# Kernel optimization log

Hardware: AMD Instinct MI355X
Metric: run time of the kernel (lower is better)

Reference implementation:

```python
import jax, jax.numpy as jnp
import numpy as np

N = 10000   # num_nodes (batch=1)
E = 160000  # num edges
CIN, H, T, OUT, K = 32, 64, 12, 12, 3


def _conv1d(x, w, b, pad):
    # x: [N, C_in, T], w: [C_out, C_in, K]
    out = jax.lax.conv_general_dilated(
        x, w, window_strides=(1,), padding=[(pad, pad)],
        dimension_numbers=('NCH', 'OIH', 'NCH'))
    return out + b[None, :, None]


def _gated_tconv(x, w, b):
    # GatedTemporalConv (dropout = identity in eval)
    out = _conv1d(x, w, b, K // 2)
    P, Q = jnp.split(out, 2, axis=1)
    return P * jax.nn.sigmoid(Q)


def _gcn(x, W, b, src, dst, ew):
    # PyG GCNConv, vectorized over all T timesteps in one fused pass.
    # x: [N, C_in, T], W: [C_out, C_in]
    xt = jnp.einsum('nct,oc->not', x, W)
    loop = jnp.arange(N)
    srcl = jnp.concatenate([src, loop])
    dstl = jnp.concatenate([dst, loop])
    ewl = jnp.concatenate([ew, jnp.ones((N,), ew.dtype)])
    deg = jax.ops.segment_sum(ewl, dstl, num_segments=N)
    dis = jnp.where(deg > 0, jax.lax.rsqrt(deg), 0.0)
    norm = dis[srcl] * ewl * dis[dstl]                      # [E+N]
    msg = xt[srcl] * norm[:, None, None]                    # [E+N, C_out, T]
    out = jax.ops.segment_sum(msg, dstl, num_segments=N)    # [N, C_out, T]
    return out + b[None, :, None]


def setup_inputs() -> dict:
    key = jax.random.key(0)
    ks = jax.random.split(key, 20)
    rn = lambda k, s: jax.random.normal(k, s, jnp.float32) * 0.05
    return {
        'x': jax.random.normal(ks[0], (N, CIN, T), jnp.float32),
        'edge_index': jax.random.randint(ks[1], (2, E), 0, N),
        'edge_weight': jax.random.uniform(ks[2], (E,), jnp.float32),
        'tc1a_w': rn(ks[3], (2 * H, CIN, K)), 'tc1a_b': rn(ks[4], (2 * H,)),
        'gc1_w': rn(ks[5], (H, H)),           'gc1_b': rn(ks[6], (H,)),
        'tc1b_w': rn(ks[7], (2 * H, H, K)),   'tc1b_b': rn(ks[8], (2 * H,)),
        'tc2a_w': rn(ks[9], (2 * H, H, K)),   'tc2a_b': rn(ks[10], (2 * H,)),
        'gc2_w': rn(ks[11], (H, H)),          'gc2_b': rn(ks[12], (H,)),
        'tc2b_w': rn(ks[13], (2 * H, H, K)),  'tc2b_b': rn(ks[14], (2 * H,)),
        'fin_w': rn(ks[15], (OUT, H, T)),     'fin_b': rn(ks[16], (OUT,)),
    }


def reference(x, edge_index, edge_weight,
              tc1a_w, tc1a_b, gc1_w, gc1_b, tc1b_w, tc1b_b,
              tc2a_w, tc2a_b, gc2_w, gc2_b, tc2b_w, tc2b_b,
              fin_w, fin_b):
    src, dst = edge_index[0], edge_index[1]
    h = _gated_tconv(x, tc1a_w, tc1a_b)
    h = jax.nn.relu(_gcn(h, gc1_w, gc1_b, src, dst, edge_weight))
    h = _gated_tconv(h, tc1b_w, tc1b_b)
    h = _gated_tconv(h, tc2a_w, tc2a_b)
    h = jax.nn.relu(_gcn(h, gc2_w, gc2_b, src, dst, edge_weight))
    h = _gated_tconv(h, tc2b_w, tc2b_b)
    h = _conv1d(h, fin_w, fin_b, 0)          # [N, OUT, 1] (kernel == T)
    h = h[:, :, 0]                            # squeeze(-1)
    return h.reshape(1, N, OUT)               # batch_size = 1
```

## Files before the change

### kernel.cpp

```cpp
#include <hip/hip_runtime.h>
#include <hip/hip_bf16.h>
#include <stdint.h>

#define N_NODES 10000
#define N_EDGES 160000
#define BUCKET 128

typedef unsigned short u16;
typedef unsigned int u32;
typedef short s16v8 __attribute__((ext_vector_type(8)));
typedef float f32v4 __attribute__((ext_vector_type(4)));

__device__ __forceinline__ float bf2f(u16 v){ return __uint_as_float(((u32)v) << 16); }
__device__ __forceinline__ u16 f2bf(float f){
    u32 u = __float_as_uint(f);
    u32 r = (u + 0x7fffu + ((u >> 16) & 1u)) >> 16;
    return (u16)r;
}

struct SmallPtrs { const void* p[14]; };

__device__ __constant__ const int g_seg_off[15] = {
    0, 12288, 12416, 16512, 16576, 41152, 41280,
    65856, 65984, 70080, 70144, 94720, 94848, 104064, 104076
};
__device__ __constant__ const int g_seg_kind[14] = {
    1, 0, 0, 0, 2, 0, 2, 0, 0, 0, 2, 0, 0, 0
};

__global__ void k_convert_init(SmallPtrs ps, u16* __restrict__ dst,
                               float* deg, int* cur){
    int i = blockIdx.x * blockDim.x + threadIdx.x;
    if (i < 104076){
        int seg = 0, base = 0;
#pragma unroll
        for (int s = 0; s < 14; s++){
            if (i >= g_seg_off[s]){ seg = s; base = g_seg_off[s]; }
        }
        int li = i - base;
        float v = ((const float*)ps.p[seg])[li];
        int kind = g_seg_kind[seg];
        int dsto = li;
        if (kind){
            int CIN = (kind == 1) ? 32 : 64;
            int o = li / (3 * CIN);
            int rem = li - o * (3 * CIN);
            int c = rem / 3, d = rem - c * 3;
            dsto = d * 128 * CIN + o * CIN + c;
        }
        dst[base + dsto] = f2bf(v);
    }
    if (i < N_NODES){ deg[i] = 1.0f; cur[i] = 0; }
}

__launch_bounds__(256, 4)
__global__ void k_gconv_count(const float* __restrict__ xin, const u16* __restrict__ wg,
                              const u16* __restrict__ bg, u16* __restrict__ out,
                              const int* __restrict__ ei, const float* __restrict__ ew,
                              float* deg, int* cur, int2* __restrict__ epack){
    if (blockIdx.x >= 1250){
        int e = (blockIdx.x - 1250) * 256 + threadIdx.x;
        if (e < N_EDGES){
            int s = ei[e];
            int d = ei[N_EDGES + e];
            float wv = ew[e];
            atomicAdd(&deg[d], wv);
            int p = atomicAdd(&cur[d], 1);
            if (p < BUCKET) epack[d * BUCKET + p] = make_int2(s, __float_as_int(wv));
        }
        return;
    }
    __shared__ __attribute__((aligned(16))) u16 shbuf[6912];
    u16* xT = shbuf;
    u16* Ho = shbuf;
    int tid = threadIdx.x;
    int n0 = blockIdx.x * 8;

    int lane = tid & 63, wave = tid >> 6;
    int col = lane & 15, quad = lane >> 4;
    int o_p = wave * 16 + col, o_q = o_p + 64;

    s16v8 Bf[3][2];
#pragma unroll
    for (int pq = 0; pq < 2; pq++){
        int o = pq ? o_q : o_p;
#pragma unroll
        for (int d = 0; d < 3; d++)
            Bf[d][pq] = *(const s16v8*)(wg + d * 4096 + o * 32 + quad * 8);
    }

    for (int i = tid; i < 8 * 40; i += 256){
        int g = i / 40, c = i % 40;
        xT[g * 560 + 0 * 40 + c] = 0; xT[g * 560 + 13 * 40 + c] = 0;
    }
    {
        int g = tid >> 5, c = tid & 31;
        const float4* p = (const float4*)(xin + ((size_t)(n0 + g) * 32 + c) * 12);
        float4 v0 = p[0], v1 = p[1], v2 = p[2];
        u16* xb = xT + g * 560 + c;
        xb[1 * 40] = f2bf(v0.x);  xb[2 * 40] = f2bf(v0.y);
        xb[3 * 40] = f2bf(v0.z);  xb[4 * 40] = f2bf(v0.w);
        xb[5 * 40] = f2bf(v1.x);  xb[6 * 40] = f2bf(v1.y);
        xb[7 * 40] = f2bf(v1.z);  xb[8 * 40] = f2bf(v1.w);
        xb[9 * 40] = f2bf(v2.x);  xb[10 * 40] = f2bf(v2.y);
        xb[11 * 40] = f2bf(v2.z); xb[12 * 40] = f2bf(v2.w);
    }
    __syncthreads();

    f32v4 aP[6], aQ[6];
#pragma unroll
    for (int mt = 0; mt < 6; mt++){ aP[mt] = (f32v4)0.f; aQ[mt] = (f32v4)0.f; }
#pragma unroll
    for (int mt = 0; mt < 6; mt++){
        int m = mt * 16 + col;
        int g = m / 12, t = m - 12 * g;
#pragma unroll
        for (int d = 0; d < 3; d++){
            s16v8 a = *(const s16v8*)&xT[g * 560 + (t + d) * 40 + quad * 8];
            aP[mt] = __builtin_amdgcn_mfma_f32_16x16x32_bf16(a, Bf[d][0], aP[mt], 0, 0, 0);
            aQ[mt] = __builtin_amdgcn_mfma_f32_16x16x32_bf16(a, Bf[d][1], aQ[mt], 0, 0, 0);
        }
    }
    __syncthreads();
    float bP = bf2f(bg[o_p]), bQ = bf2f(bg[o_q]);
#pragma unroll
    for (int mt = 0; mt < 6; mt++){
#pragma unroll
        for (int r = 0; r < 4; r++){
            int m2 = mt * 16 + quad * 4 + r;
            int g = m2 / 12, t = m2 - 12 * g;
            float pv = aP[mt][r] + bP, qv = aQ[mt][r] + bQ;
            Ho[g * 864 + t * 72 + o_p] = f2bf(pv / (1.f + __expf(-qv)));
        }
    }
    __syncthreads();
    for (int i = tid; i < 768; i += 256){
        int g = i / 96, r = i % 96, t = r / 8, ch = r % 8;
        *(s16v8*)(out + (size_t)(n0 + g) * 768 + t * 64 + ch * 8) =
            *(const s16v8*)&Ho[g * 864 + t * 72 + ch * 8];
    }
}

__global__ void k_norm(const float* __restrict__ deg, const int* __restrict__ cur,
                       int2* __restrict__ ep){
    int i = blockIdx.x * blockDim.x + threadIdx.x;
    int n = i >> 7, slot = i & 127;
    if (n >= N_NODES) return;
    int cnt = cur[n]; if (cnt > BUCKET) cnt = BUCKET;
    if (slot < cnt){
        int2 e = ep[(size_t)n * BUCKET + slot];
        float w = __int_as_float(e.y) * rsqrtf(deg[e.x]) * rsqrtf(deg[n]);
        ep[(size_t)n * BUCKET + slot].y = __float_as_int(w);
    }
}

__launch_bounds__(256, 4)
__global__ void k_gather(const u16* __restrict__ src, const float* __restrict__ deg,
                         const int* __restrict__ cur, const int2* __restrict__ ep,
                         u16* __restrict__ z){
    int slice = blockIdx.x & 7;
    int nb = blockIdx.x >> 3;
    int tid = threadIdx.x;
    int nl = tid >> 5;
    int sub = tid & 31;
    int eg = sub >> 3;
    int l8 = sub & 7;
    int n = nb * 8 + nl;
    int base = slice * 96 + l8 * 12;

    float acc[12];
    if (eg == 0){
        float sw = 1.0f / deg[n];
        const u16* xr = src + (size_t)n * 768 + base;
#pragma unroll
        for (int k = 0; k < 3; k++){
            ushort4 v = *(const ushort4*)(xr + k * 4);
            acc[k * 4 + 0] = sw * bf2f(v.x); acc[k * 4 + 1] = sw * bf2f(v.y);
            acc[k * 4 + 2] = sw * bf2f(v.z); acc[k * 4 + 3] = sw * bf2f(v.w);
        }
    } else {
#pragma unroll
        for (int k = 0; k < 12; k++) acc[k] = 0.f;
    }

    int e = cur[n]; if (e > BUCKET) e = BUCKET;
    const int2* eb = ep + (size_t)n * BUCKET;
    int p = eg;
    for (; p + 4 < e; p += 8){
        int2 e0 = eb[p], e1 = eb[p + 4];
        float w0 = __int_as_float(e0.y), w1 = __int_as_float(e1.y);
        const u16* q0 = src + (size_t)e0.x * 768 + base;
        const u16* q1 = src + (size_t)e1.x * 768 + base;
        ushort4 a0 = *(const ushort4*)(q0);
        ushort4 a1 = *(const ushort4*)(q0 + 4);
        ushort4 a2 = *(const ushort4*)(q0 + 8);
        ushort4 c0 = *(const ushort4*)(q1);
        ushort4 c1 = *(const ushort4*)(q1 + 4);
        ushort4 c2 = *(const ushort4*)(q1 + 8);
        acc[0] = fmaf(w0, bf2f(a0.x), acc[0]); acc[1] = fmaf(w0, bf2f(a0.y), acc[1]);
        acc[2] = fmaf(w0, bf2f(a0.z), acc[2]); acc[3] = fmaf(w0, bf2f(a0.w), acc[3]);
        acc[4] = fmaf(w0, bf2f(a1.x), acc[4]); acc[5] = fmaf(w0, bf2f(a1.y), acc[5]);
        acc[6] = fmaf(w0, bf2f(a1.z), acc[6]); acc[7] = fmaf(w0, bf2f(a1.w), acc[7]);
        acc[8] = fmaf(w0, bf2f(a2.x), acc[8]); acc[9] = fmaf(w0, bf2f(a2.y), acc[9]);
        acc[10] = fmaf(w0, bf2f(a2.z), acc[10]); acc[11] = fmaf(w0, bf2f(a2.w), acc[11]);
        acc[0] = fmaf(w1, bf2f(c0.x), acc[0]); acc[1] = fmaf(w1, bf2f(c0.y), acc[1]);
        acc[2] = fmaf(w1, bf2f(c0.z), acc[2]); acc[3] = fmaf(w1, bf2f(c0.w), acc[3]);
        acc[4] = fmaf(w1, bf2f(c1.x), acc[4]); acc[5] = fmaf(w1, bf2f(c1.y), acc[5]);
        acc[6] = fmaf(w1, bf2f(c1.z), acc[6]); acc[7] = fmaf(w1, bf2f(c1.w), acc[7]);
        acc[8] = fmaf(w1, bf2f(c2.x), acc[8]); acc[9] = fmaf(w1, bf2f(c2.y), acc[9]);
        acc[10] = fmaf(w1, bf2f(c2.z), acc[10]); acc[11] = fmaf(w1, bf2f(c2.w), acc[11]);
    }
    if (p < e){
        int2 e0 = eb[p];
        float w0 = __int_as_float(e0.y);
        const u16* q0 = src + (size_t)e0.x * 768 + base;
#pragma unroll
        for (int k = 0; k < 3; k++){
            ushort4 v = *(const ushort4*)(q0 + k * 4);
            acc[k * 4 + 0] = fmaf(w0, bf2f(v.x), acc[k * 4 + 0]);
            acc[k * 4 + 1] = fmaf(w0, bf2f(v.y), acc[k * 4 + 1]);
            acc[k * 4 + 2] = fmaf(w0, bf2f(v.z), acc[k * 4 + 2]);
            acc[k * 4 + 3] = fmaf(w0, bf2f(v.w), acc[k * 4 + 3]);
        }
    }
#pragma unroll
    for (int k = 0; k < 12; k++){
        acc[k] += __shfl_xor(acc[k], 8, 64);
        acc[k] += __shfl_xor(acc[k], 16, 64);
    }
    if (eg == 0){
        u16* zo = z + (size_t)n * 768 + base;
#pragma unroll
        for (int k = 0; k < 3; k++){
            ushort4 hv;
            hv.x = f2bf(acc[k * 4 + 0]); hv.y = f2bf(acc[k * 4 + 1]);
            hv.z = f2bf(acc[k * 4 + 2]); hv.w = f2bf(acc[k * 4 + 3]);
            *(ushort4*)(zo + k * 4) = hv;
        }
    }
}

#define XIDX(g, row, c) (((g) * 14 + (row)) * 72 + (c))

template<bool LAST>
__launch_bounds__(256, 4)
__global__ void k_fused(const u16* __restrict__ z,
                        const u16* __restrict__ Wmix, const u16* __restrict__ bmix,
                        const u16* __restrict__ w1, const u16* __restrict__ b1,
                        const u16* __restrict__ w2, const u16* __restrict__ b2,
                        const u16* __restrict__ fw, const u16* __restrict__ fb,
                        u16* __restrict__ outMid, float* __restrict__ outFin){
    __shared__ __attribute__((aligned(16))) u16 bufX[8 * 14 * 72];
    __shared__ __attribute__((aligned(16))) u16 bufY[8 * 14 * 72];
    int tid = threadIdx.x;
    int n0 = blockIdx.x * 8;
    int lane = tid & 63, wave = tid >> 6;
    int col = lane & 15, quad = lane >> 4;
    int o_p = wave * 16 + col, o_q = o_p + 64;

    for (int i = tid; i < 8 * 72; i += 256){
        int g = i / 72, c = i % 72;
        bufX[XIDX(g, 0, c)] = 0; bufX[XIDX(g, 13, c)] = 0;
        bufY[XIDX(g, 0, c)] = 0; bufY[XIDX(g, 13, c)] = 0;
    }
    for (int i = tid; i < 768; i += 256){
        int g = i / 96, r = i % 96, t = r >> 3, ch = r & 7;
        *(s16v8*)&bufX[XIDX(g, 1 + t, ch * 8)] =
            *(const s16v8*)(z + (size_t)(n0 + g) * 768 + t * 64 + ch * 8);
    }
    __syncthreads();

    {
        f32v4 accm[6];
#pragma unroll
        for (int mt = 0; mt < 6; mt++) accm[mt] = (f32v4)0.f;
#pragma unroll
        for (int ks = 0; ks < 2; ks++){
            s16v8 Bm = *(const s16v8*)(Wmix + (size_t)o_p * 64 + ks * 32 + quad * 8);
#pragma unroll
            for (int mt = 0; mt < 6; mt++){
                int m = mt * 16 + col;
                int g = m / 12, t = m - 12 * g;
                s16v8 a = *(const s16v8*)&bufX[XIDX(g, 1 + t, ks * 32 + quad * 8)];
                accm[mt] = __builtin_amdgcn_mfma_f32_16x16x32_bf16(a, Bm, accm[mt], 0, 0, 0);
            }
        }
        float bm = bf2f(bmix[o_p]);
#pragma unroll
        for (int mt = 0; mt < 6; mt++){
#pragma unroll
            for (int r = 0; r < 4; r++){
                int m2 = mt * 16 + quad * 4 + r;
                int g = m2 / 12, t = m2 - 12 * g;
                bufY[XIDX(g, 1 + t, o_p)] = f2bf(fmaxf(accm[mt][r] + bm, 0.f));
            }
        }
    }
    __syncthreads();

    {
        f32v4 aP[6], aQ[6];
#pragma unroll
        for (int mt = 0; mt < 6; mt++){ aP[mt] = (f32v4)0.f; aQ[mt] = (f32v4)0.f; }
#pragma unroll
        for (int ks = 0; ks < 2; ks++){
            s16v8 Bf[3][2];
#pragma unroll
            for (int pq = 0; pq < 2; pq++){
                int o = pq ? o_q : o_p;
#pragma unroll
                for (int d = 0; d < 3; d++)
                    Bf[d][pq] = *(const s16v8*)(w1 + d * 8192 + o * 64 + ks * 32 + quad * 8);
            }
#pragma unroll
            for (int mt = 0; mt < 6; mt++){
                int m = mt * 16 + col;
                int g = m / 12, t = m - 12 * g;
#pragma unroll
                for (int d = 0; d < 3; d++){
                    s16v8 a = *(const s16v8*)&bufY[XIDX(g, t + d, ks * 32 + quad * 8)];
                    aP[mt] = __builtin_amdgcn_mfma_f32_16x16x32_bf16(a, Bf[d][0], aP[mt], 0, 0, 0);
                    aQ[mt] = __builtin_amdgcn_mfma_f32_16x16x32_bf16(a, Bf[d][1], aQ[mt], 0, 0, 0);
                }
            }
        }
        float bP = bf2f(b1[o_p]), bQ = bf2f(b1[o_q]);
#pragma unroll
        for (int mt = 0; mt < 6; mt++){
#pragma unroll
            for (int r = 0; r < 4; r++){
                int m2 = mt * 16 + quad * 4 + r;
                int g = m2 / 12, t = m2 - 12 * g;
                float pv = aP[mt][r] + bP, qv = aQ[mt][r] + bQ;
                u16 hv = f2bf(pv / (1.f + __expf(-qv)));
                if (LAST) bufX[g * 1008 + o_p * 12 + t] = hv;
                else      bufX[XIDX(g, 1 + t, o_p)] = hv;
            }
        }
    }
    __syncthreads();

    if (!LAST){
        f32v4 aP[6], aQ[6];
#pragma unroll
        for (int mt = 0; mt < 6; mt++){ aP[mt] = (f32v4)0.f; aQ[mt] = (f32v4)0.f; }
#pragma unroll
        for (int ks = 0; ks < 2; ks++){
            s16v8 Bf[3][2];
#pragma unroll
            for (int pq = 0; pq < 2; pq++){
                int o = pq ? o_q : o_p;
#pragma unroll
                for (int d = 0; d < 3; d++)
                    Bf[d][pq] = *(const s16v8*)(w2 + d * 8192 + o * 64 + ks * 32 + quad * 8);
            }
#pragma unroll
            for (int mt = 0; mt < 6; mt++){
                int m = mt * 16 + col;
                int g = m / 12, t = m - 12 * g;
#pragma unroll
                for (int d = 0; d < 3; d++){
                    s16v8 a = *(const s16v8*)&bufX[XIDX(g, t + d, ks * 32 + quad * 8)];
                    aP[mt] = __builtin_amdgcn_mfma_f32_16x16x32_bf16(a, Bf[d][0], aP[mt], 0, 0, 0);
                    aQ[mt] = __builtin_amdgcn_mfma_f32_16x16x32_bf16(a, Bf[d][1], aQ[mt], 0, 0, 0);
                }
            }
        }
        float bP = bf2f(b2[o_p]), bQ = bf2f(b2[o_q]);
#pragma unroll
        for (int mt = 0; mt < 6; mt++){
#pragma unroll
            for (int r = 0; r < 4; r++){
                int m2 = mt * 16 + quad * 4 + r;
                int g = m2 / 12, t = m2 - 12 * g;
                float pv = aP[mt][r] + bP, qv = aQ[mt][r] + bQ;
                bufY[XIDX(g, 1 + t, o_p)] = f2bf(pv / (1.f + __expf(-qv)));
            }
        }
        __syncthreads();
        for (int i = tid; i < 768; i += 256){
            int g = i / 96, r = i % 96, t = r / 8, ch = r % 8;
            *(s16v8*)(outMid + (size_t)(n0 + g) * 768 + t * 64 + ch * 8) =
                *(const s16v8*)&bufY[XIDX(g, 1 + t, ch * 8)];
        }
    } else {
        if (wave == 0){
            f32v4 accF = {0.f, 0.f, 0.f, 0.f};
            int g8 = col & 7;
#pragma unroll
            for (int ks = 0; ks < 24; ks++){
                s16v8 a = *(const s16v8*)&bufX[g8 * 1008 + ks * 32 + quad * 8];
                s16v8 bfr = {0, 0, 0, 0, 0, 0, 0, 0};
                if (col < 12)
                    bfr = *(const s16v8*)(fw + (size_t)col * 768 + ks * 32 + quad * 8);
                accF = __builtin_amdgcn_mfma_f32_16x16x32_bf16(a, bfr, accF, 0, 0, 0);
            }
            if (col < 12 && quad < 2){
                float bb = bf2f(fb[col]);
#pragma unroll
                for (int r = 0; r < 4; r++){
                    int g = quad * 4 + r;
                    outFin[(size_t)(n0 + g) * 12 + col] = accF[r] + bb;
                }
            }
        }
    }
}

static inline size_t align256(size_t x){ return (x + 255) & ~(size_t)255; }

extern "C" void kernel_launch(void* const* d_in, const int* in_sizes, int n_in,
                              void* d_out, int out_size, void* d_ws, size_t ws_size,
                              hipStream_t stream){
    const float* x  = (const float*)d_in[0];
    const int* ei   = (const int*)d_in[1];
    const float* ew = (const float*)d_in[2];

    char* w = (char*)d_ws;
    u16* bufA    = (u16*)w;  w += align256((size_t)N_NODES * 768 * sizeof(u16));
    u16* bufB    = (u16*)w;  w += align256((size_t)N_NODES * 768 * sizeof(u16));
    u16* zA      = (u16*)w;  w += align256((size_t)N_NODES * 768 * sizeof(u16));
    u16* zB      = (u16*)w;  w += align256((size_t)N_NODES * 768 * sizeof(u16));
    float* deg   = (float*)w; w += align256(N_NODES * sizeof(float));
    int* cur     = (int*)w;   w += align256(N_NODES * sizeof(int));
    int2* epack  = (int2*)w;  w += align256((size_t)N_NODES * BUCKET * sizeof(int2));
    u16* cvt     = (u16*)w;   w += align256(104076 * sizeof(u16));

    u16* tc1a_w = cvt + 0;
    u16* tc1a_b = cvt + 12288;
    u16* gc1_w  = cvt + 12416;
    u16* gc1_b  = cvt + 16512;
    u16* tc1b_w = cvt + 16576;
    u16* tc1b_b = cvt + 41152;
    u16* tc2a_w = cvt + 41280;
    u16* tc2a_b = cvt + 65856;
    u16* gc2_w  = cvt + 65984;
    u16* gc2_b  = cvt + 70080;
    u16* tc2b_w = cvt + 70144;
    u16* tc2b_b = cvt + 94720;
    u16* fin_w  = cvt + 94848;
    u16* fin_b  = cvt + 104064;

    SmallPtrs ps;
    ps.p[0]  = d_in[3];  ps.p[1]  = d_in[4];
    ps.p[2]  = d_in[5];  ps.p[3]  = d_in[6];
    ps.p[4]  = d_in[7];  ps.p[5]  = d_in[8];
    ps.p[6]  = d_in[9];  ps.p[7]  = d_in[10];
    ps.p[8]  = d_in[11]; ps.p[9]  = d_in[12];
    ps.p[10] = d_in[13]; ps.p[11] = d_in[14];
    ps.p[12] = d_in[15]; ps.p[13] = d_in[16];

    k_convert_init<<<(104076 + 255) / 256, 256, 0, stream>>>(ps, cvt, deg, cur);
    k_gconv_count<<<1250 + 625, 256, 0, stream>>>(x, tc1a_w, tc1a_b, bufA, ei, ew, deg, cur, epack);
    k_norm<<<(N_NODES * BUCKET) / 256, 256, 0, stream>>>(deg, cur, epack);

    k_gather<<<1250 * 8, 256, 0, stream>>>(bufA, deg, cur, epack, zA);
    k_fused<false><<<1250, 256, 0, stream>>>(zA, gc1_w, gc1_b, tc1b_w, tc1b_b,
                                             tc2a_w, tc2a_b, nullptr, nullptr,
                                             bufB, nullptr);
    k_gather<<<1250 * 8, 256, 0, stream>>>(bufB, deg, cur, epack, zB);
    k_fused<true><<<1250, 256, 0, stream>>>(zB, gc2_w, gc2_b, tc2b_w, tc2b_b,
                                            nullptr, nullptr, fin_w, fin_b,
                                            nullptr, (float*)d_out);
}
```

Before: 230.2 us.

## Vectorize gather loads, zero-pad edge buckets, and unroll first 24 slots unconditionally

The gather kernel now loads each neighbour row slice with one 16-byte and one 8-byte load instead of three 8-byte loads, and splits each lane's 12 channels into a contiguous 8-channel part and a 4-channel part. It accumulates with packed f32x2 math and reads edge pairs as int4. k_norm zero-fills bucket slots past the degree up to 24, so the gather can run the first 24 slots unconditionally without a bounds check, which is meant to raise memory-level parallelism. The cost is extra loads of node 0 with zero weight for low-degree nodes, plus the changed element-to-lane mapping.

```diff
diff --git a/kernel.cpp b/kernel.cpp
--- a/kernel.cpp
+++ b/kernel.cpp
@@ -5,17 +5,30 @@
 #define N_NODES 10000
 #define N_EDGES 160000
 #define BUCKET 128
+#define UNROLL_SLOTS 24
 
 typedef unsigned short u16;
 typedef unsigned int u32;
 typedef short s16v8 __attribute__((ext_vector_type(8)));
 typedef float f32v4 __attribute__((ext_vector_type(4)));
+typedef float f32v2 __attribute__((ext_vector_type(2)));
+typedef unsigned int u32v4 __attribute__((ext_vector_type(4)));
+typedef unsigned int u32v2 __attribute__((ext_vector_type(2)));
 
 __device__ __forceinline__ float bf2f(u16 v){ return __uint_as_float(((u32)v) << 16); }
 __device__ __forceinline__ u16 f2bf(float f){
     u32 u = __float_as_uint(f);
     u32 r = (u + 0x7fffu + ((u >> 16) & 1u)) >> 16;
     return (u16)r;
+}
+__device__ __forceinline__ f32v2 up2(u32 v){
+    f32v2 r;
+    r.x = __uint_as_float(v << 16);
+    r.y = __uint_as_float(v & 0xffff0000u);
+    return r;
+}
+__device__ __forceinline__ u32 pk2(float lo, float hi){
+    return (u32)f2bf(lo) | ((u32)f2bf(hi) << 16);
 }
 
 struct SmallPtrs { const void* p[14]; };
@@ -151,8 +164,34 @@
         int2 e = ep[(size_t)n * BUCKET + slot];
         float w = __int_as_float(e.y) * rsqrtf(deg[e.x]) * rsqrtf(deg[n]);
         ep[(size_t)n * BUCKET + slot].y = __float_as_int(w);
-    }
-}
+    } else if (slot < UNROLL_SLOTS){
+        ep[(size_t)n * BUCKET + slot] = make_int2(0, 0);
+    }
+}
+
+#define GATHER2(P) { \
+    int4 m = *(const int4*)(eb + (P)); \
+    const u16* q0 = src + (size_t)(u32)m.x * 768; \
+    const u16* q1 = src + (size_t)(u32)m.z * 768; \
+    u32v4 a0 = *(const u32v4*)(q0 + off1); u32v2 b0 = *(const u32v2*)(q0 + off2); \
+    u32v4 a1 = *(const u32v4*)(q1 + off1); u32v2 b1 = *(const u32v2*)(q1 + off2); \
+    f32v2 w0; w0.x = __int_as_float(m.y); w0.y = w0.x; \
+    f32v2 w1; w1.x = __int_as_float(m.w); w1.y = w1.x; \
+    acc[0] += w0 * up2(a0.x); acc[1] += w0 * up2(a0.y); \
+    acc[2] += w0 * up2(a0.z); acc[3] += w0 * up2(a0.w); \
+    acc[4] += w0 * up2(b0.x); acc[5] += w0 * up2(b0.y); \
+    acc[0] += w1 * up2(a1.x); acc[1] += w1 * up2(a1.y); \
+    acc[2] += w1 * up2(a1.z); acc[3] += w1 * up2(a1.w); \
+    acc[4] += w1 * up2(b1.x); acc[5] += w1 * up2(b1.y); }
+
+#define GATHER1(P) { \
+    int2 e0 = eb[(P)]; \
+    const u16* q0 = src + (size_t)(u32)e0.x * 768; \
+    u32v4 a0 = *(const u32v4*)(q0 + off1); u32v2 b0 = *(const u32v2*)(q0 + off2); \
+    f32v2 w0; w0.x = __int_as_float(e0.y); w0.y = w0.x; \
+    acc[0] += w0 * up2(a0.x); acc[1] += w0 * up2(a0.y); \
+    acc[2] += w0 * up2(a0.z); acc[3] += w0 * up2(a0.w); \
+    acc[4] += w0 * up2(b0.x); acc[5] += w0 * up2(b0.y); }
 
 __launch_bounds__(256, 4)
 __global__ void k_gather(const u16* __restrict__ src, const float* __restrict__ deg,
@@ -166,77 +205,51 @@
     int eg = sub >> 3;
     int l8 = sub & 7;
     int n = nb * 8 + nl;
-    int base = slice * 96 + l8 * 12;
-
-    float acc[12];
+    int off1 = slice * 96 + l8 * 8;
+    int off2 = slice * 96 + 64 + l8 * 4;
+
+    f32v2 acc[6];
     if (eg == 0){
         float sw = 1.0f / deg[n];
-        const u16* xr = src + (size_t)n * 768 + base;
-#pragma unroll
-        for (int k = 0; k < 3; k++){
-            ushort4 v = *(const ushort4*)(xr + k * 4);
-            acc[k * 4 + 0] = sw * bf2f(v.x); acc[k * 4 + 1] = sw * bf2f(v.y);
-            acc[k * 4 + 2] = sw * bf2f(v.z); acc[k * 4 + 3] = sw * bf2f(v.w);
-        }
+        f32v2 swv; swv.x = sw; swv.y = sw;
+        const u16* xr = src + (size_t)n * 768;
+        u32v4 sa = *(const u32v4*)(xr + off1);
+        u32v2 sb = *(const u32v2*)(xr + off2);
+        acc[0] = swv * up2(sa.x); acc[1] = swv * up2(sa.y);
+        acc[2] = swv * up2(sa.z); acc[3] = swv * up2(sa.w);
+        acc[4] = swv * up2(sb.x); acc[5] = swv * up2(sb.y);
     } else {
 #pragma unroll
-        for (int k = 0; k < 12; k++) acc[k] = 0.f;
-    }
+        for (int k = 0; k < 6; k++) acc[k] = (f32v2)0.f;
+    }
+
+    const int2* eb = ep + (size_t)n * BUCKET;
+    GATHER2(eg * 2);
+    GATHER2(eg * 2 + 8);
+    GATHER2(eg * 2 + 16);
 
     int e = cur[n]; if (e > BUCKET) e = BUCKET;
-    const int2* eb = ep + (size_t)n * BUCKET;
-    int p = eg;
-    for (; p + 4 < e; p += 8){
-        int2 e0 = eb[p], e1 = eb[p + 4];
-        float w0 = __int_as_float(e0.y), w1 = __int_as_float(e1.y);
-        const u16* q0 = src + (size_t)e0.x * 768 + base;
-        const u16* q1 = src + (size_t)e1.x * 768 + base;
-        ushort4 a0 = *(const ushort4*)(q0);
-        ushort4 a1 = *(const ushort4*)(q0 + 4);
-        ushort4 a2 = *(const ushort4*)(q0 + 8);
-        ushort4 c0 = *(const ushort4*)(q1);
-        ushort4 c1 = *(const ushort4*)(q1 + 4);
-        ushort4 c2 = *(const ushort4*)(q1 + 8);
-        acc[0] = fmaf(w0, bf2f(a0.x), acc[0]); acc[1] = fmaf(w0, bf2f(a0.y), acc[1]);
-        acc[2] = fmaf(w0, bf2f(a0.z), acc[2]); acc[3] = fmaf(w0, bf2f(a0.w), acc[3]);
-        acc[4] = fmaf(w0, bf2f(a1.x), acc[4]); acc[5] = fmaf(w0, bf2f(a1.y), acc[5]);
-        acc[6] = fmaf(w0, bf2f(a1.z), acc[6]); acc[7] = fmaf(w0, bf2f(a1.w), acc[7]);
-        acc[8] = fmaf(w0, bf2f(a2.x), acc[8]); acc[9] = fmaf(w0, bf2f(a2.y), acc[9]);
-        acc[10] = fmaf(w0, bf2f(a2.z), acc[10]); acc[11] = fmaf(w0, bf2f(a2.w), acc[11]);
-        acc[0] = fmaf(w1, bf2f(c0.x), acc[0]); acc[1] = fmaf(w1, bf2f(c0.y), acc[1]);
-        acc[2] = fmaf(w1, bf2f(c0.z), acc[2]); acc[3] = fmaf(w1, bf2f(c0.w), acc[3]);
-        acc[4] = fmaf(w1, bf2f(c1.x), acc[4]); acc[5] = fmaf(w1, bf2f(c1.y), acc[5]);
-        acc[6] = fmaf(w1, bf2f(c1.z), acc[6]); acc[7] = fmaf(w1, bf2f(c1.w), acc[7]);
-        acc[8] = fmaf(w1, bf2f(c2.x), acc[8]); acc[9] = fmaf(w1, bf2f(c2.y), acc[9]);
-        acc[10] = fmaf(w1, bf2f(c2.z), acc[10]); acc[11] = fmaf(w1, bf2f(c2.w), acc[11]);
-    }
-    if (p < e){
-        int2 e0 = eb[p];
-        float w0 = __int_as_float(e0.y);
-        const u16* q0 = src + (size_t)e0.x * 768 + base;
-#pragma unroll
-        for (int k = 0; k < 3; k++){
-            ushort4 v = *(const ushort4*)(q0 + k * 4);
-            acc[k * 4 + 0] = fmaf(w0, bf2f(v.x), acc[k * 4 + 0]);
-            acc[k * 4 + 1] = fmaf(w0, bf2f(v.y), acc[k * 4 + 1]);
-            acc[k * 4 + 2] = fmaf(w0, bf2f(v.z), acc[k * 4 + 2]);
-            acc[k * 4 + 3] = fmaf(w0, bf2f(v.w), acc[k * 4 + 3]);
-        }
-    }
+    if (e > UNROLL_SLOTS){
+        int p = UNROLL_SLOTS + eg * 2;
+        for (; p + 1 < e; p += 8) GATHER2(p);
+        if (p < e) GATHER1(p);
+    }
+
+    float r[12];
+#pragma unroll
+    for (int j = 0; j < 6; j++){ r[2 * j] = acc[j].x; r[2 * j + 1] = acc[j].y; }
 #pragma unroll
     for (int k = 0; k < 12; k++){
-        acc[k] += __shfl_xor(acc[k], 8, 64);
-        acc[k] += __shfl_xor(acc[k], 16, 64);
+        r[k] += __shfl_xor(r[k], 8, 64);
+        r[k] += __shfl_xor(r[k], 16, 64);
     }
     if (eg == 0){
-        u16* zo = z + (size_t)n * 768 + base;
-#pragma unroll
-        for (int k = 0; k < 3; k++){
-            ushort4 hv;
-            hv.x = f2bf(acc[k * 4 + 0]); hv.y = f2bf(acc[k * 4 + 1]);
-            hv.z = f2bf(acc[k * 4 + 2]); hv.w = f2bf(acc[k * 4 + 3]);
-            *(ushort4*)(zo + k * 4) = hv;
-        }
+        u16* zo = z + (size_t)n * 768;
+        u32v4 ha; ha.x = pk2(r[0], r[1]); ha.y = pk2(r[2], r[3]);
+        ha.z = pk2(r[4], r[5]); ha.w = pk2(r[6], r[7]);
+        u32v2 hb; hb.x = pk2(r[8], r[9]); hb.y = pk2(r[10], r[11]);
+        *(u32v4*)(zo + off1) = ha;
+        *(u32v2*)(zo + off2) = hb;
     }
 }
 
```

Measured after the change: 240.2 us. 1.04x slower.
